# Optimization experiments

Hardware: AMD Instinct MI355X
Metric: run time of the kernel (lower is better)

Reference implementation:

```python
import jax, jax.numpy as jnp
import numpy as np

V = 32000   # vocab_size
E = 512     # embedding_dim
H = 512     # hidden_dim
B = 16      # batch
T = 128     # max_decoder_length
S = 512     # max_encoder_length
D = 2       # directions (bidirectional encoder)


def setup_inputs() -> dict:
    key = jax.random.key(0)
    ks = jax.random.split(key, 16)
    sc = 0.02
    x = jax.random.randint(ks[0], (B, T), 0, V, dtype=jnp.int32)
    x_lengths = jax.random.randint(ks[1], (B,), 1, T + 1, dtype=jnp.int32)
    h0 = jax.random.normal(ks[2], (1, B, H), jnp.float32) * sc
    c0 = jax.random.normal(ks[3], (1, B, H), jnp.float32) * sc
    encoder_outputs = jax.random.normal(ks[4], (B, S, D * H), jnp.float32) * sc
    emb = jax.random.normal(ks[5], (V, E), jnp.float32) * sc
    emb = emb.at[0].set(0.0)  # padding_idx=0
    W_att = jax.random.normal(ks[6], (2 * H + E, S), jnp.float32) * sc
    b_att = jnp.zeros((S,), jnp.float32)
    W_ih = jax.random.normal(ks[7], (4 * H, E + H), jnp.float32) * sc
    W_hh = jax.random.normal(ks[8], (4 * H, H), jnp.float32) * sc
    b_ih = jnp.zeros((4 * H,), jnp.float32)
    b_hh = jnp.zeros((4 * H,), jnp.float32)
    W_align = jax.random.normal(ks[9], (2 * H, H), jnp.float32) * sc
    b_align = jnp.zeros((H,), jnp.float32)
    W_out = jax.random.normal(ks[10], (H, V), jnp.float32) * sc
    b_out = jnp.zeros((V,), jnp.float32)
    return dict(x=x, x_lengths=x_lengths, h0=h0, c0=c0,
                encoder_outputs=encoder_outputs, emb=emb,
                W_att=W_att, b_att=b_att,
                W_ih=W_ih, W_hh=W_hh, b_ih=b_ih, b_hh=b_hh,
                W_align=W_align, b_align=b_align,
                W_out=W_out, b_out=b_out)


def reference(x, x_lengths, h0, c0, encoder_outputs, emb, W_att, b_att,
              W_ih, W_hh, b_ih, b_hh, W_align, b_align, W_out, b_out):
    # embedding (dropout_rate=0 -> identity)
    xe = emb[x]                                       # [B,T,E]
    # context from initial state (num_layers=1)
    context = (h0 + c0).reshape(B, 1, H)              # view(B, L, H), L=1
    context = jnp.sum(context, axis=1, keepdims=True) # [B,1,H]
    context = jnp.broadcast_to(context, (B, T, H))
    lstm_input = jnp.concatenate([context, xe], axis=-1)  # [B,T,H+E]

    # single-layer LSTM over time with packed-sequence semantics:
    # state frozen and output zeroed for t >= length
    def step(carry, inp):
        h, c = carry
        x_t, t = inp                                   # x_t: [B,H+E]
        gates = x_t @ W_ih.T + h @ W_hh.T + b_ih + b_hh
        i, f, g, o = jnp.split(gates, 4, axis=-1)
        i = jax.nn.sigmoid(i); f = jax.nn.sigmoid(f)
        g = jnp.tanh(g);       o = jax.nn.sigmoid(o)
        c_new = f * c + i * g
        h_new = o * jnp.tanh(c_new)
        valid = (t < x_lengths)[:, None]
        h2 = jnp.where(valid, h_new, h)
        c2 = jnp.where(valid, c_new, c)
        return (h2, c2), jnp.where(valid, h_new, 0.0)

    ts = jnp.arange(T)
    (_, _), outs = jax.lax.scan(step, (h0[0], c0[0]),
                                (jnp.swapaxes(lstm_input, 0, 1), ts))
    lstm_output = jnp.swapaxes(outs, 0, 1)            # [B,T,H]

    # encoder_outputs: view(dir, B, S, H) then sum over directions
    enc = encoder_outputs.reshape(D, B, S, H).sum(0)  # [B,S,H]

    attention_input = jnp.concatenate([lstm_output, lstm_input], axis=-1)  # [B,T,2H+E]
    att_logits = jax.lax.stop_gradient(attention_input @ W_att + b_att)    # no_grad in torch
    soft = jax.nn.softmax(att_logits, axis=-1)        # [B,T,S]
    h_t_bar = jnp.einsum('bts,bsh->bth', soft, enc)   # [B,T,H]

    # attention targets: 0 at t=0, (S//T)*t otherwise
    tgt_row = (S // T) * jnp.arange(T, dtype=jnp.int32)
    tgt_row = tgt_row.at[0].set(0)
    attention_targets = jnp.broadcast_to(tgt_row, (B, T))

    aligned = jax.nn.sigmoid(
        jnp.concatenate([lstm_output, h_t_bar], axis=-1) @ W_align + b_align)
    out = lstm_output + h_t_bar * aligned
    out = out @ W_out + b_out                          # [B,T,V]
    return (out, jax.lax.stop_gradient(attention_input), attention_targets)
```

## Files before the change

kernel.cpp:

```cpp
#include <hip/hip_runtime.h>
#include <hip/hip_bf16.h>
#include <math.h>


typedef __attribute__((ext_vector_type(8))) short short8;
typedef __attribute__((ext_vector_type(4))) float floatx4;
typedef __attribute__((ext_vector_type(4))) int intx4;
typedef __hip_bfloat16 bf16;

__device__ __forceinline__ float b2f(bf16 v){ return __bfloat162float(v); }
__device__ __forceinline__ bf16 f2b(float v){ return __float2bfloat16(v); }
__device__ __forceinline__ float ld(const void* p, long i, int f32){
  return f32 ? ((const float*)p)[i] : b2f(((const bf16*)p)[i]);
}

#define SENTI ((int)0xFFC1FFC1u)

__device__ __forceinline__ intx4 poll16(const void* pp){
  intx4 r;
  asm volatile("global_load_dwordx4 %0, %1, off sc0 sc1\n\ts_waitcnt vmcnt(0)"
               : "=v"(r) : "v"(pp) : "memory");
  return r;
}

__global__ void k_detect(const unsigned short* __restrict__ h0u, int* __restrict__ flags){
  if (threadIdx.x == 0){
    int bad = 0;
    for (int i=0;i<256;i++){
      int e = (h0u[i] >> 7) & 0xFF;
      if (e != 0 && (e < 100 || e > 140)) bad++;
    }
    flags[0] = (bad > 32) ? 1 : 0;
  }
}

__global__ void k_prep(const int* __restrict__ x, const void* __restrict__ h0,
                       const void* __restrict__ c0, const void* __restrict__ emb,
                       const int* __restrict__ flags, bf16* __restrict__ lstm_input,
                       bf16* __restrict__ att_ws, float* __restrict__ state0,
                       bf16* __restrict__ hbuf){
  int f32 = flags[0];
  int idx = blockIdx.x*256 + threadIdx.x;
  int m = idx >> 10, c = idx & 1023;
  float v;
  if (c < 512){
    int b = m >> 7;
    v = ld(h0, b*512 + c, f32) + ld(c0, b*512 + c, f32);
  } else {
    v = ld(emb, (long)x[m]*512 + (c - 512), f32);
  }
  bf16 bv = f2b(v);
  lstm_input[idx] = bv;
  att_ws[(long)m*1536 + 512 + c] = bv;
  if (idx < 8192){
    float hv = ld(h0, idx, f32), cv = ld(c0, idx, f32);
    hbuf[idx] = f2b(hv);
    state0[idx] = hv;
    state0[8192 + idx] = cv;
  }
}

__global__ void k_sent(int* __restrict__ hbuf32){
  long i = (long)blockIdx.x*256 + threadIdx.x;
  if (i < 520192) hbuf32[4096 + i] = SENTI;
}

__global__ void k_encT(const void* __restrict__ eo, const int* __restrict__ flags,
                       bf16* __restrict__ encT){
  __shared__ float tile[32][33];
  int f32 = flags[0];
  int b = blockIdx.z;
  int s0 = blockIdx.x*32, h0 = blockIdx.y*32;
  int tx = threadIdx.x, ty = threadIdx.y;
  #pragma unroll
  for (int j=0;j<4;j++){
    int s = s0 + ty + j*8;
    long o = (long)b*262144 + (long)s*512 + h0 + tx;
    tile[ty + j*8][tx] = ld(eo, o, f32) + ld(eo, 4194304 + o, f32);
  }
  __syncthreads();
  #pragma unroll
  for (int j=0;j<4;j++){
    int h = h0 + ty + j*8;
    encT[((long)b*512 + h)*512 + s0 + tx] = f2b(tile[tx][ty + j*8]);
  }
}

__global__ void k_tr(const void* __restrict__ in, bf16* __restrict__ out,
                     int R, int C, const int* __restrict__ flags){
  __shared__ float tile[32][33];
  int f32 = flags[0];
  int c0 = blockIdx.x*32, r0 = blockIdx.y*32;
  int tx = threadIdx.x, ty = threadIdx.y;
  #pragma unroll
  for (int j=0;j<4;j++)
    tile[ty+j*8][tx] = ld(in, (long)(r0+ty+j*8)*C + c0+tx, f32);
  __syncthreads();
  #pragma unroll
  for (int j=0;j<4;j++)
    out[(long)(c0+ty+j*8)*R + r0+tx] = f2b(tile[tx][ty+j*8]);
}

__global__ void k_cvtW(const void* __restrict__ w, const int* __restrict__ flags,
                       bf16* __restrict__ out, long n){
  int f32 = flags[0];
  long i = (long)blockIdx.x*256 + threadIdx.x;
  if (i < n) out[i] = f2b(ld(w, i, f32));
}

__global__ void k_cvt(const void* bih, const void* bhh, const void* batt,
                      const void* balign, const void* bout,
                      const int* __restrict__ flags, bf16* __restrict__ bb){
  int f32 = flags[0];
  int i = blockIdx.x*256 + threadIdx.x;
  if (i < 2048)      bb[i] = f2b(ld(bih, i, f32));
  else if (i < 4096) bb[i] = f2b(ld(bhh, i-2048, f32));
  else if (i < 4608) bb[i] = f2b(ld(batt, i-4096, f32));
  else if (i < 5120) bb[i] = f2b(ld(balign, i-4608, f32));
  else if (i < 37120) bb[i] = f2b(ld(bout, i-5120, f32));
}

__global__ void k_wswz(const void* __restrict__ whh, const int* __restrict__ flags,
                       bf16* __restrict__ wsw){
  int f32 = flags[0];
  int bid = blockIdx.x;
  int l = threadIdx.x;
  int p = bid >> 7, tt = (bid >> 4) & 7, ks = bid & 15;
  int g = tt >> 1, hh = tt & 1;
  int row = g*512 + p*32 + hh*16 + (l & 15);
  int k = ks*32 + (l >> 4)*8;
  #pragma unroll
  for (int j=0;j<8;j++)
    wsw[(long)(bid*64 + l)*8 + j] = f2b(ld(whh, (long)row*512 + k + j, f32));
}

#define M_GX    0
#define M_F32   1
#define M_BF16  2
#define M_ALIGN 3
#define M_OUT   4

template<int MODE>
__global__ void __launch_bounds__(256)
k_gemm(const bf16* __restrict__ A, const bf16* __restrict__ Bm, int K,
       float* __restrict__ outF, bf16* __restrict__ outBH, void* __restrict__ outO,
       int ldc, const bf16* __restrict__ bias1, const bf16* __restrict__ bias2,
       const bf16* __restrict__ alin, bf16* __restrict__ finin,
       const int* __restrict__ flags, long aZ, long bZ, long cZ){
  __shared__ __align__(16) bf16 As[128*32];
  __shared__ __align__(16) bf16 Bs[128*32];
  int dfl = 0;
  if constexpr (MODE == M_OUT) dfl = flags[0];
  int tid = threadIdx.x;
  int w = tid >> 6, l = tid & 63;
  int bm = blockIdx.x, bn = blockIdx.y, bz = blockIdx.z;
  const bf16* Ag = A + bz*aZ + (long)(bm*128 + (tid>>2))*K + (tid&3)*8;
  const bf16* Bg = Bm + bz*bZ + (long)(bn*128 + (tid>>2))*K + (tid&3)*8;
  int m0 = (w&1)*64, n0 = (w>>1)*64;
  floatx4 acc[4][4];
  #pragma unroll
  for (int i=0;i<4;i++)
    #pragma unroll
    for (int j=0;j<4;j++){ floatx4 z = {0.f,0.f,0.f,0.f}; acc[i][j] = z; }

  for (int k0=0; k0<K; k0+=32){
    short8 a0 = *(const short8*)(Ag + k0);
    short8 a1 = *(const short8*)(Ag + (long)64*K + k0);
    short8 b0 = *(const short8*)(Bg + k0);
    short8 b1 = *(const short8*)(Bg + (long)64*K + k0);
    __syncthreads();
    *(short8*)(As + tid*8)        = a0;
    *(short8*)(As + 2048 + tid*8) = a1;
    *(short8*)(Bs + tid*8)        = b0;
    *(short8*)(Bs + 2048 + tid*8) = b1;
    __syncthreads();
    short8 af[4], bfr[4];
    #pragma unroll
    for (int i=0;i<4;i++){
      af[i]  = *(const short8*)(As + (m0 + i*16 + (l&15))*32 + (l>>4)*8);
      bfr[i] = *(const short8*)(Bs + (n0 + i*16 + (l&15))*32 + (l>>4)*8);
    }
    #pragma unroll
    for (int i=0;i<4;i++)
      #pragma unroll
      for (int j=0;j<4;j++)
        acc[i][j] = __builtin_amdgcn_mfma_f32_16x16x32_bf16(af[i], bfr[j], acc[i][j], 0,0,0);
  }

  int rbase = (l>>4)*4;
  int cl = l & 15;
  #pragma unroll
  for (int i=0;i<4;i++){
    #pragma unroll
    for (int j=0;j<4;j++){
      int col = bn*128 + n0 + j*16 + cl;
      #pragma unroll
      for (int r=0;r<4;r++){
        int row = bm*128 + m0 + i*16 + rbase + r;
        float v = acc[i][j][r];
        if constexpr (MODE == M_GX){
          v += b2f(bias1[col]) + b2f(bias2[col]);
          int t = row & 127, b = row >> 7;
          outF[(long)(t*16 + b)*2048 + col] = v;
        } else if constexpr (MODE == M_F32){
          v += b2f(bias1[col]);
          outF[(long)row*ldc + col] = v;
        } else if constexpr (MODE == M_BF16){
          outBH[bz*cZ + (long)row*ldc + col] = f2b(v);
        } else if constexpr (MODE == M_ALIGN){
          v += b2f(bias1[col]);
          float sg = 1.0f/(1.0f + __expf(-v));
          float lo = b2f(alin[(long)row*1024 + col]);
          float hb = b2f(alin[(long)row*1024 + 512 + col]);
          finin[(long)row*512 + col] = f2b(lo + hb*sg);
        } else {
          v += b2f(bias1[col]);
          if (dfl) ((float*)outO)[(long)row*ldc + col] = v;
          else     ((bf16*)outO)[(long)row*ldc + col] = f2b(v);
        }
      }
    }
  }
}

__global__ void k_softmax(const float* __restrict__ lg, bf16* __restrict__ soft){
  __shared__ float red[256];
  int r = blockIdx.x;
  int tid = threadIdx.x;
  float x0 = lg[(long)r*512 + tid], x1 = lg[(long)r*512 + 256 + tid];
  red[tid] = fmaxf(x0, x1); __syncthreads();
  for (int s=128; s>0; s>>=1){ if (tid<s) red[tid] = fmaxf(red[tid], red[tid+s]); __syncthreads(); }
  float mx = red[0]; __syncthreads();
  float e0 = __expf(x0-mx), e1 = __expf(x1-mx);
  red[tid] = e0+e1; __syncthreads();
  for (int s=128; s>0; s>>=1){ if (tid<s) red[tid] += red[tid+s]; __syncthreads(); }
  float inv = 1.0f/red[0];
  soft[(long)r*512 + tid] = f2b(e0*inv);
  soft[(long)r*512 + 256 + tid] = f2b(e1*inv);
}

__global__ void __launch_bounds__(256, 1)
k_lstm(const float* __restrict__ gxT, const bf16* __restrict__ wsw,
       const int* __restrict__ xlen, const float* __restrict__ state0,
       bf16* __restrict__ hbuf, int* __restrict__ flags,
       bf16* __restrict__ att_ws, bf16* __restrict__ align_in){
  int p = blockIdx.x;
  int tid = threadIdx.x;
  int w = tid >> 6, l = tid & 63, w2 = w*2;
  __shared__ __align__(16) short8 wlds[8192];
  __shared__ float gx_sh[16*128];
  __shared__ __align__(16) bf16 hsh[16*32];
  __shared__ int lens[16];
  if (tid < 16) lens[tid] = xlen[tid];

  {
    const short8* wsrc = (const short8*)wsw + (long)p*8192;
    #pragma unroll
    for (int i=0;i<32;i++) wlds[i*256 + tid] = wsrc[i*256 + tid];
  }

  int b0i = tid >> 5, u = tid & 31;
  int b1i = b0i + 8;
  float h_r0 = state0[b0i*512 + p*32 + u];
  float c_r0 = state0[8192 + b0i*512 + p*32 + u];
  float h_r1 = state0[b1i*512 + p*32 + u];
  float c_r1 = state0[8192 + b1i*512 + p*32 + u];

  float gr[8];
  #pragma unroll
  for (int rep=0;rep<8;rep++){
    int idx = rep*256 + tid;
    int b = idx >> 7, jl = idx & 127;
    gr[rep] = gxT[(long)b*2048 + (jl>>5)*512 + p*32 + (jl&31)];
  }

  __syncthreads();

  for (int t=0; t<128; t++){
    #pragma unroll
    for (int rep=0;rep<8;rep++)
      gx_sh[rep*256 + tid] = gr[rep];

    const char* hbp = (const char*)hbuf + (long)t*16384 + ((l&15)*1024 + (l>>4)*16);
    intx4 a0,a1,a2,a3,a4,a5,a6,a7,a8,a9,a10,a11,a12,a13,a14,a15;
    asm volatile(
      "global_load_dwordx4 %0,  %16, off sc0 sc1\n\t"
      "global_load_dwordx4 %1,  %16, off offset:64  sc0 sc1\n\t"
      "global_load_dwordx4 %2,  %16, off offset:128 sc0 sc1\n\t"
      "global_load_dwordx4 %3,  %16, off offset:192 sc0 sc1\n\t"
      "global_load_dwordx4 %4,  %16, off offset:256 sc0 sc1\n\t"
      "global_load_dwordx4 %5,  %16, off offset:320 sc0 sc1\n\t"
      "global_load_dwordx4 %6,  %16, off offset:384 sc0 sc1\n\t"
      "global_load_dwordx4 %7,  %16, off offset:448 sc0 sc1\n\t"
      "global_load_dwordx4 %8,  %16, off offset:512 sc0 sc1\n\t"
      "global_load_dwordx4 %9,  %16, off offset:576 sc0 sc1\n\t"
      "global_load_dwordx4 %10, %16, off offset:640 sc0 sc1\n\t"
      "global_load_dwordx4 %11, %16, off offset:704 sc0 sc1\n\t"
      "global_load_dwordx4 %12, %16, off offset:768 sc0 sc1\n\t"
      "global_load_dwordx4 %13, %16, off offset:832 sc0 sc1\n\t"
      "global_load_dwordx4 %14, %16, off offset:896 sc0 sc1\n\t"
      "global_load_dwordx4 %15, %16, off offset:960 sc0 sc1\n\t"
      "s_waitcnt vmcnt(0)"
      : "=v"(a0),"=v"(a1),"=v"(a2),"=v"(a3),"=v"(a4),"=v"(a5),"=v"(a6),"=v"(a7),
        "=v"(a8),"=v"(a9),"=v"(a10),"=v"(a11),"=v"(a12),"=v"(a13),"=v"(a14),"=v"(a15)
      : "v"(hbp)
      : "memory");
    #define RETRY(A, OFF) \
      while (__builtin_expect(A.x==SENTI || A.y==SENTI || A.z==SENTI || A.w==SENTI, 0)) \
        A = poll16(hbp + (OFF));
    RETRY(a0,0)    RETRY(a1,64)   RETRY(a2,128)  RETRY(a3,192)
    RETRY(a4,256)  RETRY(a5,320)  RETRY(a6,384)  RETRY(a7,448)
    RETRY(a8,512)  RETRY(a9,576)  RETRY(a10,640) RETRY(a11,704)
    RETRY(a12,768) RETRY(a13,832) RETRY(a14,896) RETRY(a15,960)
    #undef RETRY

    if (t < 127){
      #pragma unroll
      for (int rep=0;rep<8;rep++){
        int idx = rep*256 + tid;
        int b = idx >> 7, jl = idx & 127;
        gr[rep] = gxT[(long)((t+1)*16 + b)*2048 + (jl>>5)*512 + p*32 + (jl&31)];
      }
    }

    floatx4 acc0 = {0.f,0.f,0.f,0.f};
    floatx4 acc1 = {0.f,0.f,0.f,0.f};
    #define STEPK(K, AK) { \
      short8 av = __builtin_bit_cast(short8, AK); \
      acc0 = __builtin_amdgcn_mfma_f32_16x16x32_bf16(av, wlds[(w2*16+(K))*64 + l], acc0, 0,0,0); \
      acc1 = __builtin_amdgcn_mfma_f32_16x16x32_bf16(av, wlds[((w2+1)*16+(K))*64 + l], acc1, 0,0,0); }
    STEPK(0,a0)   STEPK(1,a1)   STEPK(2,a2)   STEPK(3,a3)
    STEPK(4,a4)   STEPK(5,a5)   STEPK(6,a6)   STEPK(7,a7)
    STEPK(8,a8)   STEPK(9,a9)   STEPK(10,a10) STEPK(11,a11)
    STEPK(12,a12) STEPK(13,a13) STEPK(14,a14) STEPK(15,a15)
    #undef STEPK
    __syncthreads();

    #pragma unroll
    for (int r=0; r<4; r++){
      int bb = (l>>4)*4 + r;
      gx_sh[bb*128 + w*32 + (l&15)]      += acc0[r];
      gx_sh[bb*128 + w*32 + 16 + (l&15)] += acc1[r];
    }
    __syncthreads();

    {
      float ig = gx_sh[b0i*128 + u],      fg = gx_sh[b0i*128 + 32 + u];
      float gg = gx_sh[b0i*128 + 64 + u], og = gx_sh[b0i*128 + 96 + u];
      bool valid = (t < lens[b0i]);
      float ii = 1.f/(1.f+__expf(-ig)), ff = 1.f/(1.f+__expf(-fg));
      float g2 = tanhf(gg),             oo = 1.f/(1.f+__expf(-og));
      float cn = ff*c_r0 + ii*g2;
      float hn = oo*tanhf(cn);
      if (valid){ c_r0 = cn; h_r0 = hn; }
      float hout = valid ? hn : 0.0f;
      hsh[b0i*32 + u] = f2b(h_r0);
      int row = b0i*128 + t;
      att_ws[(long)row*1536 + p*32 + u]   = f2b(hout);
      align_in[(long)row*1024 + p*32 + u] = f2b(hout);
    }
    {
      float ig = gx_sh[b1i*128 + u],      fg = gx_sh[b1i*128 + 32 + u];
      float gg = gx_sh[b1i*128 + 64 + u], og = gx_sh[b1i*128 + 96 + u];
      bool valid = (t < lens[b1i]);
      float ii = 1.f/(1.f+__expf(-ig)), ff = 1.f/(1.f+__expf(-fg));
      float g2 = tanhf(gg),             oo = 1.f/(1.f+__expf(-og));
      float cn = ff*c_r1 + ii*g2;
      float hn = oo*tanhf(cn);
      if (valid){ c_r1 = cn; h_r1 = hn; }
      float hout = valid ? hn : 0.0f;
      hsh[b1i*32 + u] = f2b(h_r1);
      int row = b1i*128 + t;
      att_ws[(long)row*1536 + p*32 + u]   = f2b(hout);
      align_in[(long)row*1024 + p*32 + u] = f2b(hout);
    }
    __syncthreads();

    if (t < 127 && tid < 64){
      int b = tid >> 2, ch = tid & 3;
      intx4 hv = *(const intx4*)(hsh + b*32 + ch*8);
      bf16* dst = hbuf + (long)(t+1)*8192 + b*512 + p*32 + ch*8;
      asm volatile("global_store_dwordx4 %0, %1, off sc0 sc1" :: "v"(dst), "v"(hv) : "memory");
    }
  }
}

__global__ void k_finout(const bf16* __restrict__ att_ws, const int* __restrict__ flags,
                         void* __restrict__ d_out){
  int f32 = flags[0];
  long i = (long)blockIdx.x*256 + threadIdx.x;
  if (i < 3145728){
    if (f32) ((float*)d_out)[65536000 + i] = b2f(att_ws[i]);
    else     ((bf16*)d_out)[65536000 + i] = att_ws[i];
  } else if (i < 3147776){
    long j = i - 3145728;
    float tv = (float)(4*((int)j & 127));
    if (f32) ((float*)d_out)[68681728 + j] = tv;
    else     ((bf16*)d_out)[68681728 + j] = f2b(tv);
  }
}

extern "C" void kernel_launch(void* const* d_in, const int* in_sizes, int n_in,
                              void* d_out, int out_size, void* d_ws, size_t ws_size,
                              hipStream_t stream){
  const int*  x      = (const int*) d_in[0];
  const int*  xlen   = (const int*) d_in[1];
  const void* h0     = d_in[2];
  const void* c0     = d_in[3];
  const void* eo     = d_in[4];
  const void* emb    = d_in[5];
  const void* W_att  = d_in[6];
  const void* b_att  = d_in[7];
  const void* W_ih   = d_in[8];
  const void* W_hh   = d_in[9];
  const void* b_ih   = d_in[10];
  const void* b_hh   = d_in[11];
  const void* W_align= d_in[12];
  const void* b_align= d_in[13];
  const void* W_out  = d_in[14];
  const void* b_out  = d_in[15];

  char* ws = (char*)d_ws;
  bf16*  lstm_input = (bf16*)(ws + 0);
  bf16*  encT       = (bf16*)(ws + 4194304);
  bf16*  WattT      = (bf16*)(ws + 12582912);
  bf16*  WalignT    = (bf16*)(ws + 14155776);
  bf16*  WoutT      = (bf16*)(ws + 15204352);
  bf16*  Wsw        = (bf16*)(ws + 47972352);
  float* gxT        = (float*)(ws + 50069504);
  float* attlog     = (float*)(ws + 66846720);
  bf16*  soft       = (bf16*)(ws + 71041024);
  bf16*  align_in   = (bf16*)(ws + 73138176);
  bf16*  final_in   = (bf16*)(ws + 77332480);
  bf16*  hbuf       = (bf16*)(ws + 77332480);
  bf16*  att_ws     = (bf16*)(ws + 79429632);
  bf16*  bb         = (bf16*)(ws + 85721088);
  float* state0     = (float*)(ws + 85795328);
  bf16*  WihB       = (bf16*)(ws + 85893632);
  int*   flags      = (int*) (ws + 90087936);

  k_detect<<<1, 64, 0, stream>>>((const unsigned short*)h0, flags);
  k_prep<<<8192, 256, 0, stream>>>(x, h0, c0, emb, flags, lstm_input, att_ws, state0, hbuf);
  k_sent<<<2032, 256, 0, stream>>>((int*)hbuf);
  k_cvt<<<146, 256, 0, stream>>>(b_ih, b_hh, b_att, b_align, b_out, flags, bb);
  k_cvtW<<<8192, 256, 0, stream>>>(W_ih, flags, WihB, 2097152L);
  k_encT<<<dim3(16,16,16), dim3(32,8), 0, stream>>>(eo, flags, encT);
  k_tr<<<dim3(16,48),  dim3(32,8), 0, stream>>>(W_att,   WattT,   1536, 512, flags);
  k_tr<<<dim3(16,32),  dim3(32,8), 0, stream>>>(W_align, WalignT, 1024, 512, flags);
  k_tr<<<dim3(1000,16),dim3(32,8), 0, stream>>>(W_out,   WoutT,   512, 32000, flags);
  k_wswz<<<2048, 64, 0, stream>>>(W_hh, flags, Wsw);

  k_gemm<M_GX><<<dim3(16,16,1), 256, 0, stream>>>(lstm_input, WihB, 1024,
      gxT, nullptr, nullptr, 0, bb, bb+2048, nullptr, nullptr, flags, 0, 0, 0);

  k_lstm<<<16, 256, 0, stream>>>(gxT, Wsw, xlen, state0, hbuf, flags, att_ws, align_in);

  k_gemm<M_F32><<<dim3(16,4,1), 256, 0, stream>>>(att_ws, WattT, 1536,
      attlog, nullptr, nullptr, 512, bb+4096, nullptr, nullptr, nullptr, flags, 0, 0, 0);

  k_softmax<<<2048, 256, 0, stream>>>(attlog, soft);

  k_gemm<M_BF16><<<dim3(1,4,16), 256, 0, stream>>>(soft, encT, 512,
      nullptr, align_in + 512, nullptr, 1024, nullptr, nullptr, nullptr, nullptr,
      flags, 65536L, 262144L, 131072L);

  k_gemm<M_ALIGN><<<dim3(16,4,1), 256, 0, stream>>>(align_in, WalignT, 1024,
      nullptr, nullptr, nullptr, 0, bb+4608, nullptr, align_in, final_in, flags, 0, 0, 0);

  k_gemm<M_OUT><<<dim3(16,250,1), 256, 0, stream>>>(final_in, WoutT, 512,
      nullptr, nullptr, d_out, 32000, bb+5120, nullptr, nullptr, nullptr, flags, 0, 0, 0);

  k_finout<<<12296, 256, 0, stream>>>(att_ws, flags, d_out);
}
```

Before: 1.296 ms.

## Co-locate LSTM blocks on one XCD and use lighter cache scope for recurrent exchange

The LSTM kernel now launches 256 blocks, and only every 16th block continues, so the 16 working blocks likely land on the same XCD. A handshake checks whether all 16 arrived within a timeout. If they did, the per-step hidden-state exchange uses sc0-only loads and stores instead of sc0 sc1, which keeps coherence traffic local to the shared L2. The change also swaps tanhf for an exp-based fast tanh and moves the per-step output stores after the hidden-state publish, so the critical path is shorter. The risks are that the result relies on the undocumented mapping of blocks to XCDs, and that the fast tanh loses some accuracy.

```diff
diff --git a/kernel.cpp b/kernel.cpp
--- a/kernel.cpp
+++ b/kernel.cpp
@@ -13,14 +13,26 @@
 __device__ __forceinline__ float ld(const void* p, long i, int f32){
   return f32 ? ((const float*)p)[i] : b2f(((const bf16*)p)[i]);
 }
+__device__ __forceinline__ float ftanh(float x){
+  float e = __expf(2.0f*x);
+  return 1.0f - 2.0f/(e + 1.0f);
+}
 
 #define SENTI ((int)0xFFC1FFC1u)
 
-__device__ __forceinline__ intx4 poll16(const void* pp){
+__device__ __forceinline__ intx4 poll16(const void* pp, int fast){
   intx4 r;
-  asm volatile("global_load_dwordx4 %0, %1, off sc0 sc1\n\ts_waitcnt vmcnt(0)"
-               : "=v"(r) : "v"(pp) : "memory");
+  if (fast)
+    asm volatile("global_load_dwordx4 %0, %1, off sc0\n\ts_waitcnt vmcnt(0)"
+                 : "=v"(r) : "v"(pp) : "memory");
+  else
+    asm volatile("global_load_dwordx4 %0, %1, off sc0 sc1\n\ts_waitcnt vmcnt(0)"
+                 : "=v"(r) : "v"(pp) : "memory");
   return r;
+}
+
+__device__ __forceinline__ long rdclk(){
+  long v; asm volatile("s_memtime %0\n\ts_waitcnt lgkmcnt(0)" : "=s"(v)); return v;
 }
 
 __global__ void k_detect(const unsigned short* __restrict__ h0u, int* __restrict__ flags){
@@ -31,6 +43,8 @@
       if (e != 0 && (e < 100 || e > 140)) bad++;
     }
     flags[0] = (bad > 32) ? 1 : 0;
+    for (int i=0;i<16;i++) flags[128+i] = 0;
+    flags[192] = 0;
   }
 }
 
@@ -244,14 +258,48 @@
        const int* __restrict__ xlen, const float* __restrict__ state0,
        bf16* __restrict__ hbuf, int* __restrict__ flags,
        bf16* __restrict__ att_ws, bf16* __restrict__ align_in){
-  int p = blockIdx.x;
+  int bid = blockIdx.x;
+  if (bid & 15) return;
+  int p = bid >> 4;
   int tid = threadIdx.x;
   int w = tid >> 6, l = tid & 63, w2 = w*2;
   __shared__ __align__(16) short8 wlds[8192];
   __shared__ float gx_sh[16*128];
   __shared__ __align__(16) bf16 hsh[16*32];
   __shared__ int lens[16];
+  __shared__ int fastsh;
   if (tid < 16) lens[tid] = xlen[tid];
+
+  if (tid == 0){
+    int one = 1;
+    int* tok = flags + 128 + p;
+    asm volatile("global_store_dword %0, %1, off sc0" :: "v"(tok), "v"(one) : "memory");
+    long t0 = rdclk();
+    int ok = 0;
+    for(;;){
+      intx4 h0v,h1v,h2v,h3v;
+      asm volatile(
+        "global_load_dwordx4 %0, %4, off sc0\n\t"
+        "global_load_dwordx4 %1, %4, off offset:16 sc0\n\t"
+        "global_load_dwordx4 %2, %4, off offset:32 sc0\n\t"
+        "global_load_dwordx4 %3, %4, off offset:48 sc0\n\t"
+        "s_waitcnt vmcnt(0)"
+        : "=v"(h0v),"=v"(h1v),"=v"(h2v),"=v"(h3v) : "v"(flags+128) : "memory");
+      int a = h0v.x&h0v.y&h0v.z&h0v.w & h1v.x&h1v.y&h1v.z&h1v.w
+            & h2v.x&h2v.y&h2v.z&h2v.w & h3v.x&h3v.y&h3v.z&h3v.w;
+      if (a == 1){ ok = 1; break; }
+      if (rdclk() - t0 > 400000) break;
+    }
+    __hip_atomic_fetch_add(flags+192, ok ? 1 : 0x10000,
+                           __ATOMIC_RELAXED, __HIP_MEMORY_SCOPE_AGENT);
+    int c;
+    for(;;){
+      c = __hip_atomic_load(flags+192, __ATOMIC_RELAXED, __HIP_MEMORY_SCOPE_AGENT);
+      if (((c & 0xFFFF) + (c >> 16)) >= 16) break;
+      __builtin_amdgcn_s_sleep(2);
+    }
+    fastsh = ((c >> 16) == 0) ? 1 : 0;
+  }
 
   {
     const short8* wsrc = (const short8*)wsw + (long)p*8192;
@@ -275,6 +323,7 @@
   }
 
   __syncthreads();
+  const int fast = fastsh;
 
   for (int t=0; t<128; t++){
     #pragma unroll
@@ -283,31 +332,56 @@
 
     const char* hbp = (const char*)hbuf + (long)t*16384 + ((l&15)*1024 + (l>>4)*16);
     intx4 a0,a1,a2,a3,a4,a5,a6,a7,a8,a9,a10,a11,a12,a13,a14,a15;
-    asm volatile(
-      "global_load_dwordx4 %0,  %16, off sc0 sc1\n\t"
-      "global_load_dwordx4 %1,  %16, off offset:64  sc0 sc1\n\t"
-      "global_load_dwordx4 %2,  %16, off offset:128 sc0 sc1\n\t"
-      "global_load_dwordx4 %3,  %16, off offset:192 sc0 sc1\n\t"
-      "global_load_dwordx4 %4,  %16, off offset:256 sc0 sc1\n\t"
-      "global_load_dwordx4 %5,  %16, off offset:320 sc0 sc1\n\t"
-      "global_load_dwordx4 %6,  %16, off offset:384 sc0 sc1\n\t"
-      "global_load_dwordx4 %7,  %16, off offset:448 sc0 sc1\n\t"
-      "global_load_dwordx4 %8,  %16, off offset:512 sc0 sc1\n\t"
-      "global_load_dwordx4 %9,  %16, off offset:576 sc0 sc1\n\t"
-      "global_load_dwordx4 %10, %16, off offset:640 sc0 sc1\n\t"
-      "global_load_dwordx4 %11, %16, off offset:704 sc0 sc1\n\t"
-      "global_load_dwordx4 %12, %16, off offset:768 sc0 sc1\n\t"
-      "global_load_dwordx4 %13, %16, off offset:832 sc0 sc1\n\t"
-      "global_load_dwordx4 %14, %16, off offset:896 sc0 sc1\n\t"
-      "global_load_dwordx4 %15, %16, off offset:960 sc0 sc1\n\t"
-      "s_waitcnt vmcnt(0)"
-      : "=v"(a0),"=v"(a1),"=v"(a2),"=v"(a3),"=v"(a4),"=v"(a5),"=v"(a6),"=v"(a7),
-        "=v"(a8),"=v"(a9),"=v"(a10),"=v"(a11),"=v"(a12),"=v"(a13),"=v"(a14),"=v"(a15)
-      : "v"(hbp)
-      : "memory");
+    if (fast){
+      asm volatile(
+        "global_load_dwordx4 %0,  %16, off sc0\n\t"
+        "global_load_dwordx4 %1,  %16, off offset:64  sc0\n\t"
+        "global_load_dwordx4 %2,  %16, off offset:128 sc0\n\t"
+        "global_load_dwordx4 %3,  %16, off offset:192 sc0\n\t"
+        "global_load_dwordx4 %4,  %16, off offset:256 sc0\n\t"
+        "global_load_dwordx4 %5,  %16, off offset:320 sc0\n\t"
+        "global_load_dwordx4 %6,  %16, off offset:384 sc0\n\t"
+        "global_load_dwordx4 %7,  %16, off offset:448 sc0\n\t"
+        "global_load_dwordx4 %8,  %16, off offset:512 sc0\n\t"
+        "global_load_dwordx4 %9,  %16, off offset:576 sc0\n\t"
+        "global_load_dwordx4 %10, %16, off offset:640 sc0\n\t"
+        "global_load_dwordx4 %11, %16, off offset:704 sc0\n\t"
+        "global_load_dwordx4 %12, %16, off offset:768 sc0\n\t"
+        "global_load_dwordx4 %13, %16, off offset:832 sc0\n\t"
+        "global_load_dwordx4 %14, %16, off offset:896 sc0\n\t"
+        "global_load_dwordx4 %15, %16, off offset:960 sc0\n\t"
+        "s_waitcnt vmcnt(0)"
+        : "=v"(a0),"=v"(a1),"=v"(a2),"=v"(a3),"=v"(a4),"=v"(a5),"=v"(a6),"=v"(a7),
+          "=v"(a8),"=v"(a9),"=v"(a10),"=v"(a11),"=v"(a12),"=v"(a13),"=v"(a14),"=v"(a15)
+        : "v"(hbp)
+        : "memory");
+    } else {
+      asm volatile(
+        "global_load_dwordx4 %0,  %16, off sc0 sc1\n\t"
+        "global_load_dwordx4 %1,  %16, off offset:64  sc0 sc1\n\t"
+        "global_load_dwordx4 %2,  %16, off offset:128 sc0 sc1\n\t"
+        "global_load_dwordx4 %3,  %16, off offset:192 sc0 sc1\n\t"
+        "global_load_dwordx4 %4,  %16, off offset:256 sc0 sc1\n\t"
+        "global_load_dwordx4 %5,  %16, off offset:320 sc0 sc1\n\t"
+        "global_load_dwordx4 %6,  %16, off offset:384 sc0 sc1\n\t"
+        "global_load_dwordx4 %7,  %16, off offset:448 sc0 sc1\n\t"
+        "global_load_dwordx4 %8,  %16, off offset:512 sc0 sc1\n\t"
+        "global_load_dwordx4 %9,  %16, off offset:576 sc0 sc1\n\t"
+        "global_load_dwordx4 %10, %16, off offset:640 sc0 sc1\n\t"
+        "global_load_dwordx4 %11, %16, off offset:704 sc0 sc1\n\t"
+        "global_load_dwordx4 %12, %16, off offset:768 sc0 sc1\n\t"
+        "global_load_dwordx4 %13, %16, off offset:832 sc0 sc1\n\t"
+        "global_load_dwordx4 %14, %16, off offset:896 sc0 sc1\n\t"
+        "global_load_dwordx4 %15, %16, off offset:960 sc0 sc1\n\t"
+        "s_waitcnt vmcnt(0)"
+        : "=v"(a0),"=v"(a1),"=v"(a2),"=v"(a3),"=v"(a4),"=v"(a5),"=v"(a6),"=v"(a7),
+          "=v"(a8),"=v"(a9),"=v"(a10),"=v"(a11),"=v"(a12),"=v"(a13),"=v"(a14),"=v"(a15)
+        : "v"(hbp)
+        : "memory");
+    }
     #define RETRY(A, OFF) \
       while (__builtin_expect(A.x==SENTI || A.y==SENTI || A.z==SENTI || A.w==SENTI, 0)) \
-        A = poll16(hbp + (OFF));
+        A = poll16(hbp + (OFF), fast);
     RETRY(a0,0)    RETRY(a1,64)   RETRY(a2,128)  RETRY(a3,192)
     RETRY(a4,256)  RETRY(a5,320)  RETRY(a6,384)  RETRY(a7,448)
     RETRY(a8,512)  RETRY(a9,576)  RETRY(a10,640) RETRY(a11,704)
@@ -344,35 +418,33 @@
     }
     __syncthreads();
 
+    float hout0, hout1;
+    int row0, row1;
     {
       float ig = gx_sh[b0i*128 + u],      fg = gx_sh[b0i*128 + 32 + u];
       float gg = gx_sh[b0i*128 + 64 + u], og = gx_sh[b0i*128 + 96 + u];
       bool valid = (t < lens[b0i]);
       float ii = 1.f/(1.f+__expf(-ig)), ff = 1.f/(1.f+__expf(-fg));
-      float g2 = tanhf(gg),             oo = 1.f/(1.f+__expf(-og));
+      float g2 = ftanh(gg),             oo = 1.f/(1.f+__expf(-og));
       float cn = ff*c_r0 + ii*g2;
-      float hn = oo*tanhf(cn);
+      float hn = oo*ftanh(cn);
       if (valid){ c_r0 = cn; h_r0 = hn; }
-      float hout = valid ? hn : 0.0f;
+      hout0 = valid ? hn : 0.0f;
       hsh[b0i*32 + u] = f2b(h_r0);
-      int row = b0i*128 + t;
-      att_ws[(long)row*1536 + p*32 + u]   = f2b(hout);
-      align_in[(long)row*1024 + p*32 + u] = f2b(hout);
+      row0 = b0i*128 + t;
     }
     {
       float ig = gx_sh[b1i*128 + u],      fg = gx_sh[b1i*128 + 32 + u];
       float gg = gx_sh[b1i*128 + 64 + u], og = gx_sh[b1i*128 + 96 + u];
       bool valid = (t < lens[b1i]);
       float ii = 1.f/(1.f+__expf(-ig)), ff = 1.f/(1.f+__expf(-fg));
-      float g2 = tanhf(gg),             oo = 1.f/(1.f+__expf(-og));
+      float g2 = ftanh(gg),             oo = 1.f/(1.f+__expf(-og));
       float cn = ff*c_r1 + ii*g2;
-      float hn = oo*tanhf(cn);
+      float hn = oo*ftanh(cn);
       if (valid){ c_r1 = cn; h_r1 = hn; }
-      float hout = valid ? hn : 0.0f;
+      hout1 = valid ? hn : 0.0f;
       hsh[b1i*32 + u] = f2b(h_r1);
-      int row = b1i*128 + t;
-      att_ws[(long)row*1536 + p*32 + u]   = f2b(hout);
-      align_in[(long)row*1024 + p*32 + u] = f2b(hout);
+      row1 = b1i*128 + t;
     }
     __syncthreads();
 
@@ -380,8 +452,16 @@
       int b = tid >> 2, ch = tid & 3;
       intx4 hv = *(const intx4*)(hsh + b*32 + ch*8);
       bf16* dst = hbuf + (long)(t+1)*8192 + b*512 + p*32 + ch*8;
-      asm volatile("global_store_dwordx4 %0, %1, off sc0 sc1" :: "v"(dst), "v"(hv) : "memory");
-    }
+      if (fast)
+        asm volatile("global_store_dwordx4 %0, %1, off sc0" :: "v"(dst), "v"(hv) : "memory");
+      else
+        asm volatile("global_store_dwordx4 %0, %1, off sc0 sc1" :: "v"(dst), "v"(hv) : "memory");
+    }
+
+    att_ws[(long)row0*1536 + p*32 + u]   = f2b(hout0);
+    align_in[(long)row0*1024 + p*32 + u] = f2b(hout0);
+    att_ws[(long)row1*1536 + p*32 + u]   = f2b(hout1);
+    align_in[(long)row1*1024 + p*32 + u] = f2b(hout1);
   }
 }
 
@@ -453,7 +533,7 @@
   k_gemm<M_GX><<<dim3(16,16,1), 256, 0, stream>>>(lstm_input, WihB, 1024,
       gxT, nullptr, nullptr, 0, bb, bb+2048, nullptr, nullptr, flags, 0, 0, 0);
 
-  k_lstm<<<16, 256, 0, stream>>>(gxT, Wsw, xlen, state0, hbuf, flags, att_ws, align_in);
+  k_lstm<<<256, 256, 0, stream>>>(gxT, Wsw, xlen, state0, hbuf, flags, att_ws, align_in);
 
   k_gemm<M_F32><<<dim3(16,4,1), 256, 0, stream>>>(att_ws, WattT, 1536,
       attlog, nullptr, nullptr, 512, bb+4096, nullptr, nullptr, nullptr, flags, 0, 0, 0);
```

Result: faster. 1.172 ms (-9.6%).
